# Kernel tuning notes

Hardware: AMD Instinct MI355X
Metric: run time of the kernel (lower is better)

Reference implementation:

```python
import jax, jax.numpy as jnp
import numpy as np

PAD = 0
LS = 0.1          # label smoothing
END_W = 3.0       # end_weight
CHAR_W = 0.2      # char_weight
LEN_P = 0.3       # length_penalty
DIFF_MULT = 1.0   # difficulty 'easy'


def _position_weight_matrix(S):
    # Row L-1 holds the position weights for a sequence of length L,
    # replicating the Python loop in get_position_weights.
    Lf = jnp.arange(1, S + 1, dtype=jnp.float32)[:, None]   # [S,1] length
    jf = jnp.arange(S, dtype=jnp.float32)[None, :]           # [1,S] position
    Li = jnp.arange(1, S + 1)[:, None]
    ji = jnp.arange(S)[None, :]
    valid = ji < Li
    w = jnp.where(valid, 1.0 + (jf / Lf) * 0.5, 1.0)
    w = jnp.where(ji == Li - 1, END_W * 1.5, w)               # last char
    w = jnp.where((Li >= 2) & (ji == Li - 2), END_W * 1.0, w)
    w = jnp.where((Li >= 3) & (ji == Li - 3), END_W * 0.8, w)
    mid = (Li >= 4) & (ji >= Li // 3) & (ji < (2 * Li) // 3)
    w = jnp.where(mid, w * 1.3, w)
    w = jnp.where((Li <= 4) & valid, w * 1.2, w)              # short seqs
    return w


def setup_inputs() -> dict:
    key = jax.random.key(0)
    k1, k2 = jax.random.split(key)
    output = jax.random.normal(k1, (512, 128, 2048), dtype=jnp.float32)
    target = jax.random.randint(k2, (512, 128), 0, 2048)
    return {"output": output, "target": target}


def reference(output, target):
    B, S, V = output.shape
    f32 = jnp.float32
    pad_mask = target != PAD
    lens = pad_mask.sum(axis=1)                                # [B]

    # --- label-smoothed CE, ignore_index=PAD, reduction='none' ---
    logp = jax.nn.log_softmax(output, axis=-1)                 # [B,S,V]
    nll = -jnp.take_along_axis(logp, target[..., None], axis=-1)[..., 0]
    ce = (1.0 - LS) * nll + LS * (-logp.mean(axis=-1))
    ce = jnp.where(pad_mask, ce, 0.0)                          # [B,S]

    # --- position-weighted CE ---
    W = _position_weight_matrix(S)                             # [S,S]
    rows = W[jnp.clip(lens - 1, 0, S - 1)]                     # [B,S]
    pos = jnp.arange(S)[None, :]
    bw = jnp.where(pos < lens[:, None], rows, 1.0)             # [B,S]
    weighted_loss = (ce * bw).sum() / bw.sum()

    # --- length penalty ---
    preds = jnp.argmax(output, axis=-1)                        # [B,S]
    plen = (preds != PAD).sum(axis=1)
    diff = jnp.abs(plen.astype(f32) - lens.astype(f32))
    factor = 1.0 + 0.5 * (plen < lens).astype(f32) + 0.3 * (plen <= 3).astype(f32)
    length_pen = LEN_P * (diff * factor).mean()

    # --- n-gram one-hot MSE, computed analytically (exact, no [B,S,V] one-hots):
    # per position the bigram/trigram one-hots have at most one nonzero, so
    # sum_v (p*w - t*w)^2 = w^2 * (exists_p + exists_t - 2*match).
    pb = preds[:, :-1] == preds[:, 1:]                         # pred bigram exists
    tb = target[:, :-1] == target[:, 1:]
    mb = pb & tb & (preds[:, :-1] == target[:, :-1])
    bwts = jnp.where(jnp.arange(S - 1) >= S - 3, 1.5, 1.0)     # last two = 1.5
    bcnt = pb.astype(f32) + tb.astype(f32) - 2.0 * mb.astype(f32)
    bigram_loss = (bcnt * (bwts ** 2)).sum() / (B * (S - 1) * V)

    pt = pb[:, :-1] & pb[:, 1:]                                # pred trigram exists
    tt = tb[:, :-1] & tb[:, 1:]
    mt = pt & tt & (preds[:, :-2] == target[:, :-2])
    twts = jnp.where(jnp.arange(S - 2) >= S - 4, 2.0, 1.0)     # last two = 2.0
    tcnt = pt.astype(f32) + tt.astype(f32) - 2.0 * mt.astype(f32)
    trigram_loss = (tcnt * (twts ** 2)).sum() / (B * (S - 2) * V)
    any_valid = jnp.any(pad_mask[:, :-2].sum(axis=1) > 0)
    ngram_loss = bigram_loss + jnp.where(any_valid, 1.5 * trigram_loss, 0.0)

    total = DIFF_MULT * (weighted_loss * 0.7 + length_pen * 0.2 + CHAR_W * ngram_loss * 0.1)
    return total
```

## Files before the change

### kernel.cpp

```cpp
#include <hip/hip_runtime.h>
#include <math.h>

#define BB 512
#define SS 128
#define VV 2048

constexpr float LSc    = 0.1f;
constexpr float END_W  = 3.0f;
constexpr float CHAR_W = 0.2f;
constexpr float LEN_P  = 0.3f;

__global__ __launch_bounds__(256) void k_rows(const float* __restrict__ x,
                                              const int* __restrict__ tgt,
                                              float* __restrict__ ce,
                                              int* __restrict__ preds,
                                              float* __restrict__ acc,
                                              int* __restrict__ flag) {
    if (blockIdx.x == 0 && threadIdx.x == 0) {
        for (int i = 0; i < 5; ++i) acc[i] = 0.f;
        *flag = 0;
    }

    const int lane = threadIdx.x & 63;
    const int row  = blockIdx.x * 4 + (threadIdx.x >> 6);
    const float* rp = x + (size_t)row * VV;
    const int t = tgt[row];

    float4 v[8];
#pragma unroll
    for (int k = 0; k < 8; ++k)
        v[k] = *(const float4*)(rp + k * 256 + lane * 4);

    float m = v[0].x; int mi = lane * 4;
#pragma unroll
    for (int k = 0; k < 8; ++k) {
        const float f0 = v[k].x, f1 = v[k].y, f2 = v[k].z, f3 = v[k].w;
        const int base = k * 256 + lane * 4;
        if (f0 > m) { m = f0; mi = base;     }
        if (f1 > m) { m = f1; mi = base + 1; }
        if (f2 > m) { m = f2; mi = base + 2; }
        if (f3 > m) { m = f3; mi = base + 3; }
    }
#pragma unroll
    for (int off = 1; off < 64; off <<= 1) {
        float om = __shfl_xor(m, off);
        int   oi = __shfl_xor(mi, off);
        if (om > m || (om == m && oi < mi)) { m = om; mi = oi; }
    }

    float ssum = 0.f, esum = 0.f, xt = 0.f;
#pragma unroll
    for (int k = 0; k < 8; ++k) {
        const float f0 = v[k].x, f1 = v[k].y, f2 = v[k].z, f3 = v[k].w;
        const int base = k * 256 + lane * 4;
        ssum += f0 + f1 + f2 + f3;
        esum += __expf(f0 - m) + __expf(f1 - m) + __expf(f2 - m) + __expf(f3 - m);
        if (base     == t) xt = f0;
        if (base + 1 == t) xt = f1;
        if (base + 2 == t) xt = f2;
        if (base + 3 == t) xt = f3;
    }
#pragma unroll
    for (int off = 1; off < 64; off <<= 1) {
        ssum += __shfl_xor(ssum, off);
        esum += __shfl_xor(esum, off);
        xt   += __shfl_xor(xt,   off);
    }

    if (lane == 0) {
        float lse = m + logf(esum);
        float nll = lse - xt;
        float cev = (1.0f - LSc) * nll + LSc * (lse - ssum * (1.0f / VV));
        ce[row]    = (t != 0) ? cev : 0.0f;
        preds[row] = mi;
    }
}

__global__ __launch_bounds__(128) void k_batch(const int* __restrict__ tgt,
                                               const int* __restrict__ preds,
                                               const float* __restrict__ ce,
                                               float* __restrict__ acc,
                                               int* __restrict__ flag) {
    const int b = blockIdx.x;
    const int j = threadIdx.x;

    __shared__ int   st[SS];
    __shared__ int   sp[SS];
    __shared__ int   ired[128];
    __shared__ float fred[128][4];

    int   t = tgt[b * SS + j];
    int   p = preds[b * SS + j];
    float c = ce[b * SS + j];
    st[j] = t; sp[j] = p;

    ired[j] = (t != 0 ? 1 : 0) | ((p != 0 ? 1 : 0) << 8)
            | (((t != 0 && j < SS - 2) ? 1 : 0) << 16);
    __syncthreads();
    for (int off = 64; off >= 1; off >>= 1) {
        if (j < off) ired[j] += ired[j + off];
        __syncthreads();
    }
    const int r  = ired[0];
    const int L  = r & 255;
    const int P  = (r >> 8) & 255;
    const int VC = r >> 16;

    float w = 1.0f;
    if (L > 0 && j < L) {
        w = 1.0f + 0.5f * ((float)j / (float)L);
        if (j == L - 1)                w = END_W * 1.5f;
        else if (L >= 2 && j == L - 2) w = END_W * 1.0f;
        else if (L >= 3 && j == L - 3) w = END_W * 0.8f;
        if (L >= 4 && j >= L / 3 && j < (2 * L) / 3) w *= 1.3f;
        if (L <= 4) w *= 1.2f;
    }

    float big = 0.f, tri = 0.f;
    if (j < SS - 1) {
        bool pb = sp[j] == sp[j + 1];
        bool tb = st[j] == st[j + 1];
        bool mb = pb && tb && (sp[j] == st[j]);
        float wt = (j >= SS - 3) ? 2.25f : 1.0f;
        big = ((pb ? 1.f : 0.f) + (tb ? 1.f : 0.f) - 2.f * (mb ? 1.f : 0.f)) * wt;
    }
    if (j < SS - 2) {
        bool pt = (sp[j] == sp[j + 1]) && (sp[j + 1] == sp[j + 2]);
        bool tt = (st[j] == st[j + 1]) && (st[j + 1] == st[j + 2]);
        bool mt = pt && tt && (sp[j] == st[j]);
        float wt = (j >= SS - 4) ? 4.0f : 1.0f;
        tri = ((pt ? 1.f : 0.f) + (tt ? 1.f : 0.f) - 2.f * (mt ? 1.f : 0.f)) * wt;
    }

    fred[j][0] = c * w;
    fred[j][1] = w;
    fred[j][2] = big;
    fred[j][3] = tri;
    __syncthreads();
    for (int off = 64; off >= 1; off >>= 1) {
        if (j < off) {
            fred[j][0] += fred[j + off][0];
            fred[j][1] += fred[j + off][1];
            fred[j][2] += fred[j + off][2];
            fred[j][3] += fred[j + off][3];
        }
        __syncthreads();
    }
    if (j == 0) {
        atomicAdd(&acc[0], fred[0][0]);
        atomicAdd(&acc[1], fred[0][1]);
        float diff   = fabsf((float)P - (float)L);
        float factor = 1.0f + (P < L ? 0.5f : 0.f) + (P <= 3 ? 0.3f : 0.f);
        atomicAdd(&acc[2], diff * factor);
        atomicAdd(&acc[3], fred[0][2]);
        atomicAdd(&acc[4], fred[0][3]);
        if (VC > 0) atomicOr(flag, 1);
    }
}

__global__ void k_final(const float* __restrict__ acc,
                        const int* __restrict__ flag,
                        float* __restrict__ out) {
    float wl = acc[0] / acc[1];
    float lp = LEN_P * acc[2] * (1.0f / BB);
    float bg = acc[3] / (float)(BB * (SS - 1) * VV);
    float tg = acc[4] / (float)(BB * (SS - 2) * VV);
    float ng = bg + ((*flag) ? 1.5f * tg : 0.f);
    out[0] = wl * 0.7f + lp * 0.2f + CHAR_W * ng * 0.1f;
}

extern "C" void kernel_launch(void* const* d_in, const int* in_sizes, int n_in,
                              void* d_out, int out_size, void* d_ws, size_t ws_size,
                              hipStream_t stream) {
    const float* x   = (const float*)d_in[0];
    const int*   tgt = (const int*)d_in[1];
    float*       out = (float*)d_out;

    float* ce    = (float*)d_ws;
    int*   preds = (int*)((char*)d_ws + (size_t)BB * SS * 4);
    float* acc   = (float*)((char*)d_ws + (size_t)2 * BB * SS * 4);
    int*   flag  = (int*)(acc + 5);

    k_rows<<<(BB * SS) / 4, 256, 0, stream>>>(x, tgt, ce, preds, acc, flag);
    k_batch<<<BB, 128, 0, stream>>>(tgt, preds, ce, acc, flag);
    k_final<<<1, 1, 0, stream>>>(acc, flag, out);
}
```

Before: 137.6 us.

## Make row kernel persistent, load target logit directly, fuse final into batch kernel

The row kernel now launches 8192 waves that each loop over 8 rows instead of one wave per row, so there are fewer blocks to schedule. The target logit is read with one scalar load rather than compared across all elements and reduced with shuffles. The final reduction kernel is dropped: the last block of the batch kernel, found with an atomic counter, computes the output, which removes one launch. Rows inside a wave are processed one after another without explicit prefetch, so this relies on occupancy to hide memory latency.

```diff
diff --git a/kernel.cpp b/kernel.cpp
--- a/kernel.cpp
+++ b/kernel.cpp
@@ -4,6 +4,9 @@
 #define BB 512
 #define SS 128
 #define VV 2048
+#define NROWS  (BB * SS)
+#define NWAVES 8192
+#define ROWS_PER_WAVE (NROWS / NWAVES)
 
 constexpr float LSc    = 0.1f;
 constexpr float END_W  = 3.0f;
@@ -15,64 +18,64 @@
                                               float* __restrict__ ce,
                                               int* __restrict__ preds,
                                               float* __restrict__ acc,
-                                              int* __restrict__ flag) {
+                                              int* __restrict__ flagcnt) {
     if (blockIdx.x == 0 && threadIdx.x == 0) {
         for (int i = 0; i < 5; ++i) acc[i] = 0.f;
-        *flag = 0;
+        flagcnt[0] = 0;
+        flagcnt[1] = 0;
     }
 
     const int lane = threadIdx.x & 63;
-    const int row  = blockIdx.x * 4 + (threadIdx.x >> 6);
-    const float* rp = x + (size_t)row * VV;
-    const int t = tgt[row];
+    const int wid  = blockIdx.x * 4 + (threadIdx.x >> 6);
 
-    float4 v[8];
+#pragma unroll 1
+    for (int it = 0; it < ROWS_PER_WAVE; ++it) {
+        const int row = wid + it * NWAVES;
+        const float* rp = x + (size_t)row * VV;
+        const int t = tgt[row];
+        const float xt = rp[t];
+
+        float4 v[8];
 #pragma unroll
-    for (int k = 0; k < 8; ++k)
-        v[k] = *(const float4*)(rp + k * 256 + lane * 4);
+        for (int k = 0; k < 8; ++k)
+            v[k] = *(const float4*)(rp + k * 256 + lane * 4);
 
-    float m = v[0].x; int mi = lane * 4;
+        float m = v[0].x; int mi = lane * 4;
 #pragma unroll
-    for (int k = 0; k < 8; ++k) {
-        const float f0 = v[k].x, f1 = v[k].y, f2 = v[k].z, f3 = v[k].w;
-        const int base = k * 256 + lane * 4;
-        if (f0 > m) { m = f0; mi = base;     }
-        if (f1 > m) { m = f1; mi = base + 1; }
-        if (f2 > m) { m = f2; mi = base + 2; }
-        if (f3 > m) { m = f3; mi = base + 3; }
-    }
+        for (int k = 0; k < 8; ++k) {
+            const int base = k * 256 + lane * 4;
+            if (v[k].x > m) { m = v[k].x; mi = base;     }
+            if (v[k].y > m) { m = v[k].y; mi = base + 1; }
+            if (v[k].z > m) { m = v[k].z; mi = base + 2; }
+            if (v[k].w > m) { m = v[k].w; mi = base + 3; }
+        }
 #pragma unroll
-    for (int off = 1; off < 64; off <<= 1) {
-        float om = __shfl_xor(m, off);
-        int   oi = __shfl_xor(mi, off);
-        if (om > m || (om == m && oi < mi)) { m = om; mi = oi; }
-    }
+        for (int off = 1; off < 64; off <<= 1) {
+            float om = __shfl_xor(m, off);
+            int   oi = __shfl_xor(mi, off);
+            if (om > m || (om == m && oi < mi)) { m = om; mi = oi; }
+        }
 
-    float ssum = 0.f, esum = 0.f, xt = 0.f;
+        float ssum = 0.f, esum = 0.f;
 #pragma unroll
-    for (int k = 0; k < 8; ++k) {
-        const float f0 = v[k].x, f1 = v[k].y, f2 = v[k].z, f3 = v[k].w;
-        const int base = k * 256 + lane * 4;
-        ssum += f0 + f1 + f2 + f3;
-        esum += __expf(f0 - m) + __expf(f1 - m) + __expf(f2 - m) + __expf(f3 - m);
-        if (base     == t) xt = f0;
-        if (base + 1 == t) xt = f1;
-        if (base + 2 == t) xt = f2;
-        if (base + 3 == t) xt = f3;
-    }
+        for (int k = 0; k < 8; ++k) {
+            ssum += (v[k].x + v[k].y) + (v[k].z + v[k].w);
+            esum += __expf(v[k].x - m) + __expf(v[k].y - m)
+                  + __expf(v[k].z - m) + __expf(v[k].w - m);
+        }
 #pragma unroll
-    for (int off = 1; off < 64; off <<= 1) {
-        ssum += __shfl_xor(ssum, off);
-        esum += __shfl_xor(esum, off);
-        xt   += __shfl_xor(xt,   off);
-    }
+        for (int off = 1; off < 64; off <<= 1) {
+            ssum += __shfl_xor(ssum, off);
+            esum += __shfl_xor(esum, off);
+        }
 
-    if (lane == 0) {
-        float lse = m + logf(esum);
-        float nll = lse - xt;
-        float cev = (1.0f - LSc) * nll + LSc * (lse - ssum * (1.0f / VV));
-        ce[row]    = (t != 0) ? cev : 0.0f;
-        preds[row] = mi;
+        if (lane == 0) {
+            float lse = m + logf(esum);
+            float nll = lse - xt;
+            float cev = (1.0f - LSc) * nll + LSc * (lse - ssum * (1.0f / VV));
+            ce[row]    = (t != 0) ? cev : 0.0f;
+            preds[row] = mi;
+        }
     }
 }
 
@@ -80,7 +83,8 @@
                                                const int* __restrict__ preds,
                                                const float* __restrict__ ce,
                                                float* __restrict__ acc,
-                                               int* __restrict__ flag) {
+                                               int* __restrict__ flagcnt,
+                                               float* __restrict__ out) {
     const int b = blockIdx.x;
     const int j = threadIdx.x;
 
@@ -154,19 +158,26 @@
         atomicAdd(&acc[2], diff * factor);
         atomicAdd(&acc[3], fred[0][2]);
         atomicAdd(&acc[4], fred[0][3]);
-        if (VC > 0) atomicOr(flag, 1);
+        if (VC > 0) atomicOr(&flagcnt[0], 1);
+
+        __threadfence();
+        int old = __hip_atomic_fetch_add(&flagcnt[1], 1, __ATOMIC_ACQ_REL,
+                                         __HIP_MEMORY_SCOPE_AGENT);
+        if (old == BB - 1) {
+            float a0 = __hip_atomic_load(&acc[0], __ATOMIC_RELAXED, __HIP_MEMORY_SCOPE_AGENT);
+            float a1 = __hip_atomic_load(&acc[1], __ATOMIC_RELAXED, __HIP_MEMORY_SCOPE_AGENT);
+            float a2 = __hip_atomic_load(&acc[2], __ATOMIC_RELAXED, __HIP_MEMORY_SCOPE_AGENT);
+            float a3 = __hip_atomic_load(&acc[3], __ATOMIC_RELAXED, __HIP_MEMORY_SCOPE_AGENT);
+            float a4 = __hip_atomic_load(&acc[4], __ATOMIC_RELAXED, __HIP_MEMORY_SCOPE_AGENT);
+            int   fl = __hip_atomic_load(&flagcnt[0], __ATOMIC_RELAXED, __HIP_MEMORY_SCOPE_AGENT);
+            float wl = a0 / a1;
+            float lp = LEN_P * a2 * (1.0f / BB);
+            float bg = a3 / (float)(BB * (SS - 1) * VV);
+            float tg = a4 / (float)(BB * (SS - 2) * VV);
+            float ng = bg + (fl ? 1.5f * tg : 0.f);
+            out[0] = wl * 0.7f + lp * 0.2f + CHAR_W * ng * 0.1f;
+        }
     }
-}
-
-__global__ void k_final(const float* __restrict__ acc,
-                        const int* __restrict__ flag,
-                        float* __restrict__ out) {
-    float wl = acc[0] / acc[1];
-    float lp = LEN_P * acc[2] * (1.0f / BB);
-    float bg = acc[3] / (float)(BB * (SS - 1) * VV);
-    float tg = acc[4] / (float)(BB * (SS - 2) * VV);
-    float ng = bg + ((*flag) ? 1.5f * tg : 0.f);
-    out[0] = wl * 0.7f + lp * 0.2f + CHAR_W * ng * 0.1f;
 }
 
 extern "C" void kernel_launch(void* const* d_in, const int* in_sizes, int n_in,
@@ -176,12 +187,11 @@
     const int*   tgt = (const int*)d_in[1];
     float*       out = (float*)d_out;
 
-    float* ce    = (float*)d_ws;
-    int*   preds = (int*)((char*)d_ws + (size_t)BB * SS * 4);
-    float* acc   = (float*)((char*)d_ws + (size_t)2 * BB * SS * 4);
-    int*   flag  = (int*)(acc + 5);
+    float* ce      = (float*)d_ws;
+    int*   preds   = (int*)((char*)d_ws + (size_t)NROWS * 4);
+    float* acc     = (float*)((char*)d_ws + (size_t)2 * NROWS * 4);
+    int*   flagcnt = (int*)(acc + 5);
 
-    k_rows<<<(BB * SS) / 4, 256, 0, stream>>>(x, tgt, ce, preds, acc, flag);
-    k_batch<<<BB, 128, 0, stream>>>(tgt, preds, ce, acc, flag);
-    k_final<<<1, 1, 0, stream>>>(acc, flag, out);
+    k_rows<<<NWAVES / 4, 256, 0, stream>>>(x, tgt, ce, preds, acc, flagcnt);
+    k_batch<<<BB, 128, 0, stream>>>(tgt, preds, ce, acc, flagcnt, out);
 }
```

After: 157.9 us. +14.7%, slower.
